# Kernel tuning notes

Hardware: AMD Instinct MI355X
Metric: run time of the kernel (lower is better)

## Reference

```python
import jax, jax.numpy as jnp
import numpy as np

EMB = 1024
NHEAD = 16
DILATIONS = (1, 4, 8, 16)
KSIZE = 7
ROT_DIM = 32  # RotaryEmbedding(dim=32): only first 32 channels of each head rotated


def neighbor_idx(T, k, d):
    # NATTEN-style 1D dilated neighborhood: window of k positions on the
    # dilation lattice (same residue class mod d), centered and clamped at borders.
    i = jnp.arange(T)
    r = i % d                      # residue class
    p = i // d                     # position within class
    Lr = (T - r + d - 1) // d      # class length
    s = jnp.clip(p - k // 2, 0, Lr - k)
    j = jnp.arange(k)
    return r[:, None] + (s[:, None] + j[None, :]) * d  # [T, k] int indices


def rope(x, rot_dim=ROT_DIM):
    # lucidrains RotaryEmbedding.rotate_queries_or_keys: interleaved pairs,
    # applied over seq dim (-2), only first rot_dim channels.
    T = x.shape[-2]
    inv = 1.0 / (10000.0 ** (jnp.arange(0, rot_dim, 2, dtype=jnp.float32) / rot_dim))
    freqs = jnp.arange(T, dtype=jnp.float32)[:, None] * inv[None, :]  # [T, rot_dim//2]
    freqs = jnp.repeat(freqs, 2, axis=-1)                             # [T, rot_dim]
    cos, sin = jnp.cos(freqs), jnp.sin(freqs)
    xr, xp = x[..., :rot_dim], x[..., rot_dim:]
    x1, x2 = xr[..., 0::2], xr[..., 1::2]
    rot = jnp.stack([-x2, x1], axis=-1).reshape(xr.shape)
    return jnp.concatenate([xr * cos + rot * sin, xp], axis=-1)


def setup_inputs() -> dict:
    key = jax.random.key(0)
    ks = jax.random.split(key, 5)
    B, T, C = 4, 8192, EMB
    s = 0.02
    return {
        "x": jax.random.normal(ks[0], (B, T, C), jnp.float32),
        "wq": jax.random.normal(ks[1], (C, C), jnp.float32) * s,
        "bq": jnp.zeros((C,), jnp.float32),
        "wk": jax.random.normal(ks[2], (C, C), jnp.float32) * s,
        "bk": jnp.zeros((C,), jnp.float32),
        "wv": jax.random.normal(ks[3], (C, C), jnp.float32) * s,
        "bv": jnp.zeros((C,), jnp.float32),
        "wp": jax.random.normal(ks[4], (C, C), jnp.float32) * s,
        "bp": jnp.zeros((C,), jnp.float32),
    }


def reference(x, wq, bq, wk, bk, wv, bv, wp, bp):
    B, T, C = x.shape
    hs = C // NHEAD

    def heads(w, b):  # torch Linear: x @ W^T + b, then [B, nh, T, hs]
        return (x @ w.T + b).reshape(B, T, NHEAD, hs).transpose(0, 2, 1, 3)

    q, k, v = heads(wq, bq), heads(wk, bk), heads(wv, bv)
    present = jnp.stack([k, v])  # pre-rotary kv cache, as in original

    q, k, v = rope(q), rope(k), rope(v)  # original also rotates v

    gsz = NHEAD // len(DILATIONS)
    outs = []
    for gi, d in enumerate(DILATIONS):
        sl = slice(gi * gsz, (gi + 1) * gsz)
        idx = neighbor_idx(T, KSIZE, d)           # [T, K]
        kk = k[:, sl][:, :, idx]                   # [B, g, T, K, hs]
        vv = v[:, sl][:, :, idx]                   # [B, g, T, K, hs]
        scores = jnp.einsum('bgtd,bgtkd->bgtk', q[:, sl], kk)  # no 1/sqrt(hs), as na1d_qk
        attn = jax.nn.softmax(scores, axis=-1)
        outs.append(jnp.einsum('bgtk,bgtkd->bgtd', attn, vv))
    y = jnp.concatenate(outs, axis=1)              # [B, nh, T, hs]
    y = y.transpose(0, 2, 1, 3).reshape(B, T, C)
    y = y @ wp.T + bp
    return (y, present)
```

## Files before the change

kernel.cpp:

```cpp
#include <hip/hip_runtime.h>

typedef unsigned short ushortT;
typedef unsigned int uint32;
typedef __attribute__((ext_vector_type(8))) short short8;
typedef __attribute__((ext_vector_type(4))) float f32x4;

__device__ __forceinline__ ushortT f2bf(float f) {
    uint32 u = __float_as_uint(f);
    uint32 r = (u + 0x7fffu + ((u >> 16) & 1u)) >> 16;
    return (ushortT)r;
}
__device__ __forceinline__ float bf2f(uint32 v) {
    return __uint_as_float(v << 16);
}

__device__ __forceinline__ void unpack8(uint4 v, float* f) {
    f[0] = bf2f(v.x & 0xffffu); f[1] = bf2f(v.x >> 16);
    f[2] = bf2f(v.y & 0xffffu); f[3] = bf2f(v.y >> 16);
    f[4] = bf2f(v.z & 0xffffu); f[5] = bf2f(v.z >> 16);
    f[6] = bf2f(v.w & 0xffffu); f[7] = bf2f(v.w >> 16);
}

typedef __attribute__((address_space(1))) const void gvoid;
typedef __attribute__((address_space(3))) void lvoid;
__device__ __forceinline__ void gld16(const ushortT* g, ushortT* l) {
    __builtin_amdgcn_global_load_lds((gvoid*)g, (lvoid*)l, 16, 0, 0);
}

__global__ __launch_bounds__(256) void f32_to_bf16_kernel(
    const float* __restrict__ src, ushortT* __restrict__ dst, int n4)
{
    int i = blockIdx.x * 256 + threadIdx.x;
    if (i < n4) {
        float4 v = reinterpret_cast<const float4*>(src)[i];
        ushort4 o;
        o.x = f2bf(v.x); o.y = f2bf(v.y); o.z = f2bf(v.z); o.w = f2bf(v.w);
        reinterpret_cast<ushort4*>(dst)[i] = o;
    }
}

__global__ __launch_bounds__(256) void wconv_kernel(
    const float* __restrict__ s0, const float* __restrict__ s1,
    const float* __restrict__ s2, const float* __restrict__ s3,
    ushortT* __restrict__ dst)
{
    int i = blockIdx.x * 256 + threadIdx.x;
    const int wsel = i >> 18;
    const int off  = i & 262143;
    const float* s = (wsel == 0) ? s0 : (wsel == 1 ? s1 : (wsel == 2 ? s2 : s3));
    float4 v = reinterpret_cast<const float4*>(s)[off];
    ushort4 o;
    o.x = f2bf(v.x); o.y = f2bf(v.y); o.z = f2bf(v.z); o.w = f2bf(v.w);
    reinterpret_cast<ushort4*>(dst)[i] = o;
}

__global__ __launch_bounds__(256) void pack_bias_kernel(
    const float* __restrict__ bq, const float* __restrict__ bk,
    const float* __restrict__ bv, float* __restrict__ out)
{
    int i = blockIdx.x * 256 + threadIdx.x;
    float v = (i < 1024) ? bq[i] : (i < 2048 ? bk[i - 1024] : bv[i - 2048]);
    out[i] = v;
}

__global__ __launch_bounds__(256) void rope_table_kernel(float2* __restrict__ tab)
{
    int idx = blockIdx.x * 256 + threadIdx.x;
    int t = idx >> 4;
    int i = idx & 15;
    float inv = powf(10000.0f, -(float)i / 16.0f);
    float ang = (float)t * inv;
    tab[idx] = make_float2(cosf(ang), sinf(ang));
}

__device__ __forceinline__ short8 ldsfrag(const ushortT* region, int row, int g) {
    int e = (row << 5) + (g << 3);
    e ^= ((row >> 1) & 3) << 3;
    return *reinterpret_cast<const short8*>(region + e);
}

#define MC_ ((size_t)33554432)

template<int MODE>
__global__ __launch_bounds__(512, 4) void gemm_wide_kernel(
    const ushortT* __restrict__ A,
    const ushortT* __restrict__ Wall,
    const float*   __restrict__ biasAll,
    const float2*  __restrict__ tab,
    ushortT*       __restrict__ CbAll,
    float*         __restrict__ CfAll,
    int M, int N, int K)
{
    __shared__ ushortT lds[2 * 12288];
    const int tid  = threadIdx.x;
    const int lane = tid & 63;
    const int wv   = tid >> 6;
    const int wm   = wv >> 1;
    const int wn   = wv & 1;
    const int g    = lane >> 4;
    const int rsel = lane & 15;

    const int bidAll = blockIdx.x;
    const int proj   = (MODE == 3) ? (bidAll >> 10) : 0;
    const int bid    = (MODE == 3) ? (bidAll & 1023) : bidAll;

    const ushortT* W    = Wall + (size_t)proj * 1024 * K;
    const float*   bias = biasAll + proj * 1024;

    const int xi  = bid & 7;
    const int j   = bid >> 3;
    const int tn  = j & 7;
    const int tm  = xi * 16 + (j >> 3);
    const int m0  = tm * 256, n0 = tn * 128;

    const int crow = tid >> 2;
    const int ccol = ((tid & 3) ^ ((tid >> 3) & 3)) * 8;
    const ushortT* gA0 = A + (size_t)(m0 + crow) * K + ccol;
    const ushortT* gA1 = gA0 + (size_t)128 * K;
    const ushortT* gB0 = W + (size_t)(n0 + crow) * K + ccol;

    const int dA0 = wv * 512;
    const int dA1 = 4096 + wv * 512;
    const int dB  = 8192 + wv * 512;

    #define STAGE(buf, t) { \
        ushortT* b_ = lds + (buf) * 12288; \
        gld16(gA0 + (t) * 32, b_ + dA0); \
        gld16(gA1 + (t) * 32, b_ + dA1); \
        gld16(gB0 + (t) * 32, b_ + dB); \
    }

    f32x4 acc[4][4] = {};
    const int NT = K >> 5;
    int cur = 0;

    STAGE(0, 0);

    #pragma unroll 1
    for (int t = 0; t < NT; ++t) {
        __syncthreads();
        if (t + 1 < NT) STAGE(cur ^ 1, t + 1);

        const ushortT* ra = lds + cur * 12288;
        const ushortT* rb = ra + 8192;
        short8 Af[4], Bf[4];
        #pragma unroll
        for (int fm = 0; fm < 4; ++fm) Af[fm] = ldsfrag(ra, wm * 64 + fm * 16 + rsel, g);
        #pragma unroll
        for (int fn = 0; fn < 4; ++fn) Bf[fn] = ldsfrag(rb, wn * 64 + fn * 16 + rsel, g);
        #pragma unroll
        for (int fm = 0; fm < 4; ++fm)
            #pragma unroll
            for (int fn = 0; fn < 4; ++fn)
                acc[fm][fn] = __builtin_amdgcn_mfma_f32_16x16x32_bf16(Af[fm], Bf[fn], acc[fm][fn], 0, 0, 0);
        cur ^= 1;
    }
    #undef STAGE

    #pragma unroll
    for (int fn = 0; fn < 4; ++fn) {
        const int colb = n0 + wn * 64 + fn * 16 + rsel;
        const int d    = colb & 63;
        const float bv = bias[colb];
        #pragma unroll
        for (int fm = 0; fm < 4; ++fm) {
            const int rowbase = m0 + wm * 64 + fm * 16 + g * 4;
            #pragma unroll
            for (int e = 0; e < 4; ++e) {
                const int row = rowbase + e;
                const float val = acc[fm][fn][e] + bv;
                if (MODE == 2) {
                    CfAll[(size_t)row * N + colb] = val;
                } else {
                    if (proj != 0) {
                        const int b = row >> 13, t = row & 8191;
                        const int h = colb >> 6;
                        CfAll[(size_t)(proj - 1) * MC_ +
                              (((size_t)b * 16 + h) * 8192 + t) * 64 + d] = val;
                    }
                    const float pv = __shfl_xor(val, 1, 64);
                    float ov = val;
                    if (d < 32) {
                        const int t = row & 8191;
                        const float2 cs = tab[t * 16 + (d >> 1)];
                        ov = (d & 1) ? fmaf(val, cs.x,  pv * cs.y)
                                     : fmaf(val, cs.x, -pv * cs.y);
                    }
                    CbAll[(size_t)proj * MC_ + (size_t)row * 1024 + colb] = f2bf(ov);
                }
            }
        }
    }
}

__global__ __launch_bounds__(256) void natt_kernel(
    const ushortT* __restrict__ Q,
    const ushortT* __restrict__ Kl,
    const ushortT* __restrict__ Vl,
    ushortT*       __restrict__ O)
{
    const int T = 8192;
    const int tid  = threadIdx.x;
    const int lane = tid & 63;
    const int tloc = lane >> 3;
    const int c    = lane & 7;

    const int sbid = (blockIdx.x & 7) * 2048 + (blockIdx.x >> 3);
    const int wq   = sbid * 4 + (tid >> 6);
    const int qidx = wq * 8 + tloc;
    const int t = qidx & (T - 1);
    const int h = (qidx >> 13) & 15;
    const int b = qidx >> 17;

    const int shifts[4] = {0, 2, 3, 4};
    const int sh = shifts[h >> 2];
    const int dd = 1 << sh;

    const int r  = t & (dd - 1);
    const int p  = t >> sh;
    const int Lr = ((T - 1 - r) >> sh) + 1;
    int s = p - 3;
    const int smax = Lr - 7;
    s = s < 0 ? 0 : (s > smax ? smax : s);
    const int tbase = r + (s << sh);

    const size_t qoff = ((size_t)(b * T + t)) * 1024 + h * 64 + c * 8;
    float qf[8];
    unpack8(*reinterpret_cast<const uint4*>(Q + qoff), qf);

    const size_t cbase = ((size_t)b * T) * 1024 + h * 64 + c * 8;

    float sc[7];
    #pragma unroll
    for (int j = 0; j < 7; ++j) {
        const int tj = tbase + (j << sh);
        float kf[8];
        unpack8(*reinterpret_cast<const uint4*>(Kl + cbase + (size_t)tj * 1024), kf);
        float pp = 0.f;
        #pragma unroll
        for (int i = 0; i < 8; ++i) pp = fmaf(qf[i], kf[i], pp);
        pp += __shfl_xor(pp, 1, 64);
        pp += __shfl_xor(pp, 2, 64);
        pp += __shfl_xor(pp, 4, 64);
        sc[j] = pp;
    }

    float mx = sc[0];
    #pragma unroll
    for (int j = 1; j < 7; ++j) mx = fmaxf(mx, sc[j]);
    float den = 0.f;
    #pragma unroll
    for (int j = 0; j < 7; ++j) { sc[j] = __expf(sc[j] - mx); den += sc[j]; }
    const float inv = 1.0f / den;

    float out[8] = {};
    #pragma unroll
    for (int j = 0; j < 7; ++j) {
        const int tj = tbase + (j << sh);
        float vf[8];
        unpack8(*reinterpret_cast<const uint4*>(Vl + cbase + (size_t)tj * 1024), vf);
        #pragma unroll
        for (int i = 0; i < 8; ++i) out[i] = fmaf(sc[j], vf[i], out[i]);
    }

    short8 ov;
    #pragma unroll
    for (int i = 0; i < 8; ++i) ov[i] = (short)f2bf(out[i] * inv);
    *reinterpret_cast<short8*>(const_cast<ushortT*>(O + qoff)) = ov;
}

extern "C" void kernel_launch(void* const* d_in, const int* in_sizes, int n_in,
                              void* d_out, int out_size, void* d_ws, size_t ws_size,
                              hipStream_t stream)
{
    const float* x  = (const float*)d_in[0];
    const float* wq = (const float*)d_in[1];
    const float* bq = (const float*)d_in[2];
    const float* wk = (const float*)d_in[3];
    const float* bk = (const float*)d_in[4];
    const float* wv = (const float*)d_in[5];
    const float* bv = (const float*)d_in[6];
    const float* wp = (const float*)d_in[7];
    const float* bp = (const float*)d_in[8];

    const int B = 4, T = 8192, C = 1024;
    const int M = B * T;
    const size_t MC = (size_t)M * C;

    char* ws = (char*)d_ws;
    ushortT* xb    = (ushortT*)ws;
    ushortT* wallb = (ushortT*)(ws + (size_t)64 * 1024 * 1024);
    ushortT* wpb   = wallb + (size_t)3 * C * C;
    ushortT* qlin  = (ushortT*)(ws + (size_t)72 * 1024 * 1024);
    ushortT* klin  = qlin + MC;
    ushortT* vlin  = klin + MC;
    float2*  tab   = (float2*)(ws + (size_t)264 * 1024 * 1024);
    float*   bqkv  = (float*)(ws + (size_t)266 * 1024 * 1024);

    float* y     = (float*)d_out;
    float* presK = y + MC;

    rope_table_kernel<<<512, 256, 0, stream>>>(tab);
    pack_bias_kernel<<<12, 256, 0, stream>>>(bq, bk, bv, bqkv);

    f32_to_bf16_kernel<<<(int)(MC / 4 / 256), 256, 0, stream>>>(x, xb, (int)(MC / 4));
    wconv_kernel<<<4 * (C * C / 4) / 256, 256, 0, stream>>>(wq, wk, wv, wp, wallb);

    gemm_wide_kernel<3><<<3072, 512, 0, stream>>>(
        xb, wallb, bqkv, tab, qlin, presK, M, C, C);

    natt_kernel<<<(B * 16 * T) / 32, 256, 0, stream>>>(qlin, klin, vlin, xb);

    gemm_wide_kernel<2><<<1024, 512, 0, stream>>>(
        xb, wpb, bp, tab, nullptr, y, M, C, C);
}
```

Baseline: 569.1 us.

## Rewrite GEMM as 256x256 tile with deeper LDS pipeline and interleaved scheduling

Replaces the 256x128-tile double-buffered GEMM with a 256x256-tile kernel that uses 128 KB of dynamic LDS. Loads run several k-substeps ahead under explicit vmcnt waits, and LDS fragment reads and MFMA bursts are interleaved with barriers and setprio hints. The larger tile raises operand reuse per LDS byte and the manual schedule aims to overlap global loads with compute. In exchange occupancy drops to 2 blocks per CU, the unrolled loop hardcodes K=1024, and register pressure from 32 accumulators rises.

```diff
diff --git a/kernel.cpp b/kernel.cpp
--- a/kernel.cpp
+++ b/kernel.cpp
@@ -73,16 +73,57 @@
     tab[idx] = make_float2(cosf(ang), sinf(ang));
 }
 
-__device__ __forceinline__ short8 ldsfrag(const ushortT* region, int row, int g) {
-    int e = (row << 5) + (g << 3);
-    e ^= ((row >> 1) & 3) << 3;
-    return *reinterpret_cast<const short8*>(region + e);
-}
-
 #define MC_ ((size_t)33554432)
 
+
+#define STAGEU(tile, kk) { \
+    ushortT* la_ = lds + ((tile) & 1) * 16384 + (kk) * 8192 + wv * 512; \
+    ushortT* lb_ = la_ + 32768; \
+    const ushortT* ga_ = pA + (tile) * 64 + (kk) * 32; \
+    const ushortT* gb_ = pB + (tile) * 64 + (kk) * 32; \
+    gld16(ga_, la_); gld16(ga_ + (size_t)128 * K, la_ + 4096); \
+    gld16(gb_, lb_); gld16(gb_ + (size_t)128 * K, lb_ + 4096); }
+
+#define RDA(s, kk, rfh) { \
+    const ushortT* ra_ = lds + (s) * 16384 + (kk) * 8192 + aoff + (rfh) * 2048; \
+    Af0 = *reinterpret_cast<const short8*>(ra_); \
+    Af1 = *reinterpret_cast<const short8*>(ra_ + 512); \
+    Af2 = *reinterpret_cast<const short8*>(ra_ + 1024); \
+    Af3 = *reinterpret_cast<const short8*>(ra_ + 1536); }
+
+#define RDB(s, kk) { \
+    const ushortT* rb_ = lds + (s) * 16384 + (kk) * 8192 + boff; \
+    Bf0 = *reinterpret_cast<const short8*>(rb_); \
+    Bf1 = *reinterpret_cast<const short8*>(rb_ + 512); \
+    Bf2 = *reinterpret_cast<const short8*>(rb_ + 1024); \
+    Bf3 = *reinterpret_cast<const short8*>(rb_ + 1536); }
+
+#define SYNCA \
+    __builtin_amdgcn_s_barrier(); \
+    asm volatile("s_waitcnt lgkmcnt(0)" ::: "memory"); \
+    __builtin_amdgcn_sched_barrier(0);
+
+#define MM1(RF, CF, AF, BF) \
+    acc[RF][CF] = __builtin_amdgcn_mfma_f32_16x16x32_bf16(AF, BF, acc[RF][CF], 0, 0, 0);
+
+#define MMQ(RFH) \
+    __builtin_amdgcn_s_setprio(1); \
+    MM1((RFH)*4+0, 0, Af0, Bf0) MM1((RFH)*4+0, 1, Af0, Bf1) \
+    MM1((RFH)*4+0, 2, Af0, Bf2) MM1((RFH)*4+0, 3, Af0, Bf3) \
+    MM1((RFH)*4+1, 0, Af1, Bf0) MM1((RFH)*4+1, 1, Af1, Bf1) \
+    MM1((RFH)*4+1, 2, Af1, Bf2) MM1((RFH)*4+1, 3, Af1, Bf3) \
+    MM1((RFH)*4+2, 0, Af2, Bf0) MM1((RFH)*4+2, 1, Af2, Bf1) \
+    MM1((RFH)*4+2, 2, Af2, Bf2) MM1((RFH)*4+2, 3, Af2, Bf3) \
+    MM1((RFH)*4+3, 0, Af3, Bf0) MM1((RFH)*4+3, 1, Af3, Bf1) \
+    MM1((RFH)*4+3, 2, Af3, Bf2) MM1((RFH)*4+3, 3, Af3, Bf3) \
+    __builtin_amdgcn_s_setprio(0); \
+    __builtin_amdgcn_s_barrier();
+
+#define VM4 asm volatile("s_waitcnt vmcnt(4)" ::: "memory");
+#define VM0 asm volatile("s_waitcnt vmcnt(0)" ::: "memory");
+
 template<int MODE>
-__global__ __launch_bounds__(512, 4) void gemm_wide_kernel(
+__global__ __launch_bounds__(512, 2) void gemm8_kernel(
     const ushortT* __restrict__ A,
     const ushortT* __restrict__ Wall,
     const float*   __restrict__ biasAll,
@@ -91,84 +132,84 @@
     float*         __restrict__ CfAll,
     int M, int N, int K)
 {
-    __shared__ ushortT lds[2 * 12288];
+    extern __shared__ ushortT lds[];
     const int tid  = threadIdx.x;
     const int lane = tid & 63;
     const int wv   = tid >> 6;
-    const int wm   = wv >> 1;
-    const int wn   = wv & 1;
+    const int wm   = wv >> 2;
+    const int wn   = wv & 3;
     const int g    = lane >> 4;
     const int rsel = lane & 15;
 
     const int bidAll = blockIdx.x;
-    const int proj   = (MODE == 3) ? (bidAll >> 10) : 0;
-    const int bid    = (MODE == 3) ? (bidAll & 1023) : bidAll;
+    const int proj   = (MODE == 3) ? (bidAll >> 9) : 0;
+    const int bid    = (MODE == 3) ? (bidAll & 511) : bidAll;
 
     const ushortT* W    = Wall + (size_t)proj * 1024 * K;
     const float*   bias = biasAll + proj * 1024;
 
-    const int xi  = bid & 7;
-    const int j   = bid >> 3;
-    const int tn  = j & 7;
-    const int tm  = xi * 16 + (j >> 3);
-    const int m0  = tm * 256, n0 = tn * 128;
-
-    const int crow = tid >> 2;
-    const int ccol = ((tid & 3) ^ ((tid >> 3) & 3)) * 8;
-    const ushortT* gA0 = A + (size_t)(m0 + crow) * K + ccol;
-    const ushortT* gA1 = gA0 + (size_t)128 * K;
-    const ushortT* gB0 = W + (size_t)(n0 + crow) * K + ccol;
-
-    const int dA0 = wv * 512;
-    const int dA1 = 4096 + wv * 512;
-    const int dB  = 8192 + wv * 512;
-
-    #define STAGE(buf, t) { \
-        ushortT* b_ = lds + (buf) * 12288; \
-        gld16(gA0 + (t) * 32, b_ + dA0); \
-        gld16(gA1 + (t) * 32, b_ + dA1); \
-        gld16(gB0 + (t) * 32, b_ + dB); \
-    }
-
-    f32x4 acc[4][4] = {};
-    const int NT = K >> 5;
-    int cur = 0;
-
-    STAGE(0, 0);
+    const int xi = bid & 7;
+    const int jb = bid >> 3;
+    const int tn = jb & 3;
+    const int tm = xi * 16 + (jb >> 2);
+    const int m0 = tm * 256, n0 = tn * 256;
+
+    const int g0 = (tid & 3) ^ ((tid >> 3) & 3);
+    const ushortT* pA = A + (size_t)(m0 + (tid >> 2)) * K + g0 * 8;
+    const ushortT* pB = W + (size_t)(n0 + (tid >> 2)) * K + g0 * 8;
+
+    const int gsw  = g ^ ((rsel >> 1) & 3);
+    const int aoff = (wm * 128 + rsel) * 32 + gsw * 8;
+    const int boff = 32768 + (wn * 64 + rsel) * 32 + gsw * 8;
+
+    f32x4 acc[8][4] = {};
+    short8 Af0, Af1, Af2, Af3, Bf0, Bf1, Bf2, Bf3;
+
+    STAGEU(0, 0);
+    STAGEU(0, 1);
+    STAGEU(1, 0);
+    VM4;
+    __builtin_amdgcn_s_barrier();
 
     #pragma unroll 1
-    for (int t = 0; t < NT; ++t) {
-        __syncthreads();
-        if (t + 1 < NT) STAGE(cur ^ 1, t + 1);
-
-        const ushortT* ra = lds + cur * 12288;
-        const ushortT* rb = ra + 8192;
-        short8 Af[4], Bf[4];
-        #pragma unroll
-        for (int fm = 0; fm < 4; ++fm) Af[fm] = ldsfrag(ra, wm * 64 + fm * 16 + rsel, g);
-        #pragma unroll
-        for (int fn = 0; fn < 4; ++fn) Bf[fn] = ldsfrag(rb, wn * 64 + fn * 16 + rsel, g);
-        #pragma unroll
-        for (int fm = 0; fm < 4; ++fm)
-            #pragma unroll
-            for (int fn = 0; fn < 4; ++fn)
-                acc[fm][fn] = __builtin_amdgcn_mfma_f32_16x16x32_bf16(Af[fm], Bf[fn], acc[fm][fn], 0, 0, 0);
-        cur ^= 1;
-    }
-    #undef STAGE
-
-    #pragma unroll
-    for (int fn = 0; fn < 4; ++fn) {
-        const int colb = n0 + wn * 64 + fn * 16 + rsel;
+    for (int j = 0; j < 8; ++j) {
+        const int t0 = 2 * j;
+        RDA(0, 0, 0); RDB(0, 0);
+        STAGEU(t0 + 1, 1);
+        SYNCA; MMQ(0);
+        RDA(0, 0, 1);
+        SYNCA; MMQ(1);
+        RDA(0, 1, 0); RDB(0, 1);
+        if (j < 7) { STAGEU(t0 + 2, 0); }
+        SYNCA; MMQ(0);
+        RDA(0, 1, 1);
+        if (j < 7) { VM4 } else { VM0 }
+        SYNCA; MMQ(1);
+        RDA(1, 0, 0); RDB(1, 0);
+        if (j < 7) { STAGEU(t0 + 2, 1); }
+        SYNCA; MMQ(0);
+        RDA(1, 0, 1);
+        SYNCA; MMQ(1);
+        RDA(1, 1, 0); RDB(1, 1);
+        if (j < 7) { STAGEU(t0 + 3, 0); }
+        SYNCA; MMQ(0);
+        RDA(1, 1, 1);
+        if (j < 7) { VM4 }
+        SYNCA; MMQ(1);
+    }
+
+    #pragma unroll
+    for (int cf = 0; cf < 4; ++cf) {
+        const int colb = n0 + wn * 64 + cf * 16 + rsel;
         const int d    = colb & 63;
         const float bv = bias[colb];
         #pragma unroll
-        for (int fm = 0; fm < 4; ++fm) {
-            const int rowbase = m0 + wm * 64 + fm * 16 + g * 4;
+        for (int rf = 0; rf < 8; ++rf) {
+            const int rowbase = m0 + wm * 128 + rf * 16 + g * 4;
             #pragma unroll
             for (int e = 0; e < 4; ++e) {
                 const int row = rowbase + e;
-                const float val = acc[fm][fn][e] + bv;
+                const float val = acc[rf][cf][e] + bv;
                 if (MODE == 2) {
                     CfAll[(size_t)row * N + colb] = val;
                 } else {
@@ -300,17 +341,22 @@
     float* y     = (float*)d_out;
     float* presK = y + MC;
 
+    hipFuncSetAttribute((const void*)gemm8_kernel<3>,
+                        hipFuncAttributeMaxDynamicSharedMemorySize, 131072);
+    hipFuncSetAttribute((const void*)gemm8_kernel<2>,
+                        hipFuncAttributeMaxDynamicSharedMemorySize, 131072);
+
     rope_table_kernel<<<512, 256, 0, stream>>>(tab);
     pack_bias_kernel<<<12, 256, 0, stream>>>(bq, bk, bv, bqkv);
 
     f32_to_bf16_kernel<<<(int)(MC / 4 / 256), 256, 0, stream>>>(x, xb, (int)(MC / 4));
     wconv_kernel<<<4 * (C * C / 4) / 256, 256, 0, stream>>>(wq, wk, wv, wp, wallb);
 
-    gemm_wide_kernel<3><<<3072, 512, 0, stream>>>(
+    gemm8_kernel<3><<<1536, 512, 131072, stream>>>(
         xb, wallb, bqkv, tab, qlin, presK, M, C, C);
 
     natt_kernel<<<(B * 16 * T) / 32, 256, 0, stream>>>(qlin, klin, vlin, xb);
 
-    gemm_wide_kernel<2><<<1024, 512, 0, stream>>>(
+    gemm8_kernel<2><<<512, 512, 131072, stream>>>(
         xb, wpb, bp, tab, nullptr, y, M, C, C);
 }
```

Result: slower. 597.0 us (+4.9%).
